# Optimization experiments

Hardware: AMD Instinct MI355X
Metric: run time of the kernel (lower is better)

Reference implementation:

```python
import jax, jax.numpy as jnp
import numpy as np

BETA = 0.001  # commitment loss weight from __init__ default


def setup_inputs() -> dict:
    key = jax.random.key(0)
    k1, k2 = jax.random.split(key)
    N, INPUT_DIM = 8192, 1024
    S, K, D = 32, 1024, 32  # nsplits, num_embeddings, embedding_dim
    z = jax.random.normal(k1, (N, INPUT_DIM), dtype=jnp.float32)
    # Stacked codebook weights: one [K, D] embedding table per split.
    W = jax.random.normal(k2, (S, K, D), dtype=jnp.float32)
    return {"z": z, "W": W}


def reference(z, W):
    N, INPUT_DIM = z.shape
    S, K, D = W.shape
    zc = z.reshape(N, S, D)  # per-split chunks, matches torch.chunk(z, S, -1)
    # Squared euclidean distances ||z||^2 + ||w||^2 - 2 z.w  -> [N, S, K]
    d2 = (
        jnp.sum(zc * zc, axis=-1, keepdims=True)
        + jnp.sum(W * W, axis=-1)[None, :, :]
        - 2.0 * jnp.einsum("nsd,skd->nsk", zc, W)
    )
    idx = jnp.argmin(d2, axis=-1)  # [N, S]
    # Gather nearest codes: W[s, idx[n, s]] -> [N, S, D]
    zq = W[jnp.arange(S)[None, :], idx]
    # Sum over splits of per-split mse means; equal split sizes so this is
    # S * mean over the whole tensor.
    sg = jax.lax.stop_gradient
    loss = S * (
        jnp.mean((sg(zq) - zc) ** 2) + BETA * jnp.mean((zq - sg(zc)) ** 2)
    )
    # Straight-through estimator
    zq_st = zc + sg(zq - zc)
    return zq_st.reshape(N, INPUT_DIM), loss
```

## Files before the change

kernel.cpp:

```cpp
#include <hip/hip_runtime.h>
#include <math.h>

#define NN 8192
#define SS 32
#define DD 32
#define KK 1024
#define OUT_ELEMS ((size_t)NN * SS * DD)

#define LOSS_SCALE (32.0f * 1.001f / 8388608.0f)

typedef _Float16 half8 __attribute__((ext_vector_type(8)));
typedef float   floatx4 __attribute__((ext_vector_type(4)));


__global__ __launch_bounds__(256) void vq_prep(const float* __restrict__ W,
                                               _Float16* __restrict__ wh,
                                               _Float16* __restrict__ wl,
                                               float* __restrict__ w2,
                                               float* __restrict__ out) {
    const int g    = blockIdx.x * 256 + threadIdx.x;
    const int row  = g >> 2;
    const int part = g & 3;
    const float* wr = W + (size_t)row * DD + part * 8;
    const float4 a = ((const float4*)wr)[0];
    const float4 b = ((const float4*)wr)[1];
    float ps = 0.0f;
    ps = fmaf(a.x, a.x, ps); ps = fmaf(a.y, a.y, ps);
    ps = fmaf(a.z, a.z, ps); ps = fmaf(a.w, a.w, ps);
    ps = fmaf(b.x, b.x, ps); ps = fmaf(b.y, b.y, ps);
    ps = fmaf(b.z, b.z, ps); ps = fmaf(b.w, b.w, ps);
    ps += __shfl_xor(ps, 1, 64);
    ps += __shfl_xor(ps, 2, 64);
    if (part == 0) w2[row] = ps;

    const float src[8] = {a.x, a.y, a.z, a.w, b.x, b.y, b.z, b.w};
    half8 h, l;
    #pragma unroll
    for (int j = 0; j < 8; ++j) {
        const _Float16 hv = (_Float16)src[j];
        h[j] = hv;
        l[j] = (_Float16)(src[j] - (float)hv);
    }
    *(half8*)(wh + (size_t)row * DD + part * 8) = h;
    *(half8*)(wl + (size_t)row * DD + part * 8) = l;
    if (g == 0) out[OUT_ELEMS] = 0.0f;
}

#define RG 4

__global__ __launch_bounds__(256, 4) void vq_mfma(const float* __restrict__ z,
                                                  const float* __restrict__ W,
                                                  const _Float16* __restrict__ wh,
                                                  const _Float16* __restrict__ wl,
                                                  const float* __restrict__ w2,
                                                  float* __restrict__ out) {
    __shared__ float lds_w2[KK + 16];
    __shared__ int   lds_idx[4][64];

    const int s    = blockIdx.x & (SS - 1);
    const int n0b  = (blockIdx.x >> 5) * 256;
    const int tid  = threadIdx.x;
    const int wv   = tid >> 6;
    const int lane = tid & 63;
    const int col  = lane & 15;
    const int quad = lane >> 4;

    const float* w2s = w2 + (size_t)s * KK;
    #pragma unroll
    for (int j = 0; j < 4; ++j) lds_w2[tid + j * 256] = w2s[tid + j * 256];
    __syncthreads();

    const int n0w = n0b + wv * 64;

    half8 zh[RG], zl[RG];
    #pragma unroll
    for (int rg = 0; rg < RG; ++rg) {
        const float* zp = z + (size_t)(n0w + rg * 16 + col) * (SS * DD) + s * DD + quad * 8;
        const float4 va = ((const float4*)zp)[0];
        const float4 vb = ((const float4*)zp)[1];
        const float src[8] = {va.x, va.y, va.z, va.w, vb.x, vb.y, vb.z, vb.w};
        #pragma unroll
        for (int j = 0; j < 8; ++j) {
            const float v = -2.0f * src[j];
            const _Float16 h = (_Float16)v;
            zh[rg][j] = h;
            zl[rg][j] = (_Float16)(v - (float)h);
        }
    }

    const _Float16* whs = wh + ((size_t)s * KK + col) * DD + quad * 8;
    const _Float16* wls = wl + ((size_t)s * KK + col) * DD + quad * 8;

    floatx4 best[RG];
    int bi[RG][4];
    #pragma unroll
    for (int rg = 0; rg < RG; ++rg) {
        best[rg] = (floatx4){INFINITY, INFINITY, INFINITY, INFINITY};
        bi[rg][0] = bi[rg][1] = bi[rg][2] = bi[rg][3] = 0;
    }

    half8 bh = *(const half8*)(whs);
    half8 bl = *(const half8*)(wls);
    float wv2 = lds_w2[col];

    for (int t = 0; t < KK / 16; ++t) {
        const half8 bh_n = *(const half8*)(whs + (size_t)(t + 1) * 16 * DD);
        const half8 bl_n = *(const half8*)(wls + (size_t)(t + 1) * 16 * DD);
        const float wv2_n = lds_w2[(t + 1) * 16 + col];

        #pragma unroll
        for (int rg = 0; rg < RG; ++rg) {
            floatx4 acc = {wv2, wv2, wv2, wv2};
            acc = __builtin_amdgcn_mfma_f32_16x16x32_f16(zh[rg], bh, acc, 0, 0, 0);
            acc = __builtin_amdgcn_mfma_f32_16x16x32_f16(zl[rg], bh, acc, 0, 0, 0);
            acc = __builtin_amdgcn_mfma_f32_16x16x32_f16(zh[rg], bl, acc, 0, 0, 0);
            #pragma unroll
            for (int i = 0; i < 4; ++i) {
                if (acc[i] < best[rg][i]) { best[rg][i] = acc[i]; bi[rg][i] = t; }
            }
        }
        bh = bh_n; bl = bl_n; wv2 = wv2_n;
    }

    #pragma unroll
    for (int rg = 0; rg < RG; ++rg) {
        #pragma unroll
        for (int i = 0; i < 4; ++i) {
            float v = best[rg][i];
            int   k = bi[rg][i] * 16 + col;
            #pragma unroll
            for (int m = 1; m < 16; m <<= 1) {
                const float vo = __shfl_xor(v, m, 64);
                const int   ko = __shfl_xor(k, m, 64);
                if (vo < v || (vo == v && ko < k)) { v = vo; k = ko; }
            }
            if (col == 0) lds_idx[wv][rg * 16 + quad * 4 + i] = k;
        }
    }
    __syncthreads();

    const int krow = lds_idx[wv][lane];
    const float* wsrc = W + ((size_t)s * KK + krow) * DD;
    const size_t zoff = (size_t)(n0w + lane) * (SS * DD) + s * DD;
    const float* zsrc = z + zoff;
    float* od = out + zoff;
    float sq = 0.0f;
    #pragma unroll
    for (int c = 0; c < 8; ++c) {
        const float4 wq = ((const float4*)wsrc)[c];
        const float4 zv = ((const float4*)zsrc)[c];
        const float d0 = wq.x - zv.x, d1 = wq.y - zv.y;
        const float d2 = wq.z - zv.z, d3 = wq.w - zv.w;
        sq = fmaf(d0, d0, sq); sq = fmaf(d1, d1, sq);
        sq = fmaf(d2, d2, sq); sq = fmaf(d3, d3, sq);
        ((float4*)od)[c] = wq;
    }
    #pragma unroll
    for (int off = 32; off > 0; off >>= 1) sq += __shfl_down(sq, off, 64);
    if (lane == 0) atomicAdd(out + OUT_ELEMS, sq * LOSS_SCALE);
}

extern "C" void kernel_launch(void* const* d_in, const int* in_sizes, int n_in,
                              void* d_out, int out_size, void* d_ws, size_t ws_size,
                              hipStream_t stream) {
    const float* z = (const float*)d_in[0];
    const float* W = (const float*)d_in[1];
    float* out = (float*)d_out;

    _Float16* wh = (_Float16*)d_ws;
    _Float16* wl = wh + (size_t)SS * KK * DD;
    float*    w2 = (float*)(wl + (size_t)SS * KK * DD);

    vq_prep<<<dim3((SS * KK * 4) / 256), dim3(256), 0, stream>>>(W, wh, wl, w2, out);
    vq_mfma<<<dim3((NN / 256) * SS), dim3(256), 0, stream>>>(z, W, wh, wl, w2, out);
}
```

Before: 176.9 us.

## Fuse codebook fp16 split conversion into main kernel with LDS double buffering

Removes the separate prep kernel and performs the fp16 hi/lo split and squared-norm computation on the fly inside the main kernel. Each block stages 64-code chunks through double-buffered shared memory, so the four waves share one conversion per chunk, and a barrier follows each chunk. The loss accumulator is now zeroed with a memset. This drops one launch and the workspace round trip. In exchange, every block redoes the conversion of its split's codebook, each chunk adds a barrier, and the occupancy hint falls from 4 to 2 blocks.

Result: no change. 174.5 us (-1.3%).

```diff
diff --git a/kernel.cpp b/kernel.cpp
--- a/kernel.cpp
+++ b/kernel.cpp
@@ -12,50 +12,17 @@
 typedef _Float16 half8 __attribute__((ext_vector_type(8)));
 typedef float   floatx4 __attribute__((ext_vector_type(4)));
 
+#define CH_TILES 4
+#define CHUNK_K  (CH_TILES * 16)
+#define NCHUNK   (KK / CHUNK_K)
 
-__global__ __launch_bounds__(256) void vq_prep(const float* __restrict__ W,
-                                               _Float16* __restrict__ wh,
-                                               _Float16* __restrict__ wl,
-                                               float* __restrict__ w2,
-                                               float* __restrict__ out) {
-    const int g    = blockIdx.x * 256 + threadIdx.x;
-    const int row  = g >> 2;
-    const int part = g & 3;
-    const float* wr = W + (size_t)row * DD + part * 8;
-    const float4 a = ((const float4*)wr)[0];
-    const float4 b = ((const float4*)wr)[1];
-    float ps = 0.0f;
-    ps = fmaf(a.x, a.x, ps); ps = fmaf(a.y, a.y, ps);
-    ps = fmaf(a.z, a.z, ps); ps = fmaf(a.w, a.w, ps);
-    ps = fmaf(b.x, b.x, ps); ps = fmaf(b.y, b.y, ps);
-    ps = fmaf(b.z, b.z, ps); ps = fmaf(b.w, b.w, ps);
-    ps += __shfl_xor(ps, 1, 64);
-    ps += __shfl_xor(ps, 2, 64);
-    if (part == 0) w2[row] = ps;
-
-    const float src[8] = {a.x, a.y, a.z, a.w, b.x, b.y, b.z, b.w};
-    half8 h, l;
-    #pragma unroll
-    for (int j = 0; j < 8; ++j) {
-        const _Float16 hv = (_Float16)src[j];
-        h[j] = hv;
-        l[j] = (_Float16)(src[j] - (float)hv);
-    }
-    *(half8*)(wh + (size_t)row * DD + part * 8) = h;
-    *(half8*)(wl + (size_t)row * DD + part * 8) = l;
-    if (g == 0) out[OUT_ELEMS] = 0.0f;
-}
-
-#define RG 4
-
-__global__ __launch_bounds__(256, 4) void vq_mfma(const float* __restrict__ z,
-                                                  const float* __restrict__ W,
-                                                  const _Float16* __restrict__ wh,
-                                                  const _Float16* __restrict__ wl,
-                                                  const float* __restrict__ w2,
-                                                  float* __restrict__ out) {
-    __shared__ float lds_w2[KK + 16];
-    __shared__ int   lds_idx[4][64];
+__global__ __launch_bounds__(256, 2) void vq_fused(const float* __restrict__ z,
+                                                   const float* __restrict__ W,
+                                                   float* __restrict__ out) {
+    __shared__ _Float16 bufH[2][CH_TILES][64][8];
+    __shared__ _Float16 bufL[2][CH_TILES][64][8];
+    __shared__ float    w2b[2][CHUNK_K];
+    __shared__ int      lds_idx[4][64];
 
     const int s    = blockIdx.x & (SS - 1);
     const int n0b  = (blockIdx.x >> 5) * 256;
@@ -65,16 +32,12 @@
     const int col  = lane & 15;
     const int quad = lane >> 4;
 
-    const float* w2s = w2 + (size_t)s * KK;
-    #pragma unroll
-    for (int j = 0; j < 4; ++j) lds_w2[tid + j * 256] = w2s[tid + j * 256];
-    __syncthreads();
-
+    const float* __restrict__ Ws = W + (size_t)s * KK * DD;
     const int n0w = n0b + wv * 64;
 
-    half8 zh[RG], zl[RG];
+    half8 zh[4], zl[4];
     #pragma unroll
-    for (int rg = 0; rg < RG; ++rg) {
+    for (int rg = 0; rg < 4; ++rg) {
         const float* zp = z + (size_t)(n0w + rg * 16 + col) * (SS * DD) + s * DD + quad * 8;
         const float4 va = ((const float4*)zp)[0];
         const float4 vb = ((const float4*)zp)[1];
@@ -88,42 +51,87 @@
         }
     }
 
-    const _Float16* whs = wh + ((size_t)s * KK + col) * DD + quad * 8;
-    const _Float16* wls = wl + ((size_t)s * KK + col) * DD + quad * 8;
+    const float* __restrict__ stg = Ws + ((size_t)(wv * 16 + col)) * DD + quad * 8;
 
-    floatx4 best[RG];
-    int bi[RG][4];
+    floatx4 best[4];
+    int bi[4][4];
     #pragma unroll
-    for (int rg = 0; rg < RG; ++rg) {
+    for (int rg = 0; rg < 4; ++rg) {
         best[rg] = (floatx4){INFINITY, INFINITY, INFINITY, INFINITY};
         bi[rg][0] = bi[rg][1] = bi[rg][2] = bi[rg][3] = 0;
     }
 
-    half8 bh = *(const half8*)(whs);
-    half8 bl = *(const half8*)(wls);
-    float wv2 = lds_w2[col];
+    float4 pa = ((const float4*)stg)[0];
+    float4 pb = ((const float4*)stg)[1];
+    {
+        const float src[8] = {pa.x, pa.y, pa.z, pa.w, pb.x, pb.y, pb.z, pb.w};
+        half8 h8, l8; float ps = 0.0f;
+        #pragma unroll
+        for (int j = 0; j < 8; ++j) {
+            const float v = src[j];
+            ps = fmaf(v, v, ps);
+            const _Float16 h = (_Float16)v;
+            h8[j] = h;
+            l8[j] = (_Float16)(v - (float)h);
+        }
+        ps += __shfl_xor(ps, 16, 64);
+        ps += __shfl_xor(ps, 32, 64);
+        *(half8*)&bufH[0][wv][lane][0] = h8;
+        *(half8*)&bufL[0][wv][lane][0] = l8;
+        if (quad == 0) w2b[0][wv * 16 + col] = ps;
+    }
+    __syncthreads();
 
-    for (int t = 0; t < KK / 16; ++t) {
-        const half8 bh_n = *(const half8*)(whs + (size_t)(t + 1) * 16 * DD);
-        const half8 bl_n = *(const half8*)(wls + (size_t)(t + 1) * 16 * DD);
-        const float wv2_n = lds_w2[(t + 1) * 16 + col];
+    for (int c = 0; c < NCHUNK; ++c) {
+        const int b = c & 1;
+        if (c + 1 < NCHUNK) {
+            const float* nsrc = stg + (size_t)(c + 1) * CHUNK_K * DD;
+            pa = ((const float4*)nsrc)[0];
+            pb = ((const float4*)nsrc)[1];
+        }
 
         #pragma unroll
-        for (int rg = 0; rg < RG; ++rg) {
-            floatx4 acc = {wv2, wv2, wv2, wv2};
-            acc = __builtin_amdgcn_mfma_f32_16x16x32_f16(zh[rg], bh, acc, 0, 0, 0);
-            acc = __builtin_amdgcn_mfma_f32_16x16x32_f16(zl[rg], bh, acc, 0, 0, 0);
-            acc = __builtin_amdgcn_mfma_f32_16x16x32_f16(zh[rg], bl, acc, 0, 0, 0);
+        for (int tt = 0; tt < CH_TILES; ++tt) {
+            const half8 bh = *(const half8*)&bufH[b][tt][lane][0];
+            const half8 bl = *(const half8*)&bufL[b][tt][lane][0];
+            const float wv2 = w2b[b][tt * 16 + col];
+            const floatx4 c0 = {wv2, wv2, wv2, wv2};
+            const int tk = c * CH_TILES + tt;
             #pragma unroll
-            for (int i = 0; i < 4; ++i) {
-                if (acc[i] < best[rg][i]) { best[rg][i] = acc[i]; bi[rg][i] = t; }
+            for (int rg = 0; rg < 4; ++rg) {
+                floatx4 acc = __builtin_amdgcn_mfma_f32_16x16x32_f16(zh[rg], bh, c0, 0, 0, 0);
+                acc = __builtin_amdgcn_mfma_f32_16x16x32_f16(zl[rg], bh, acc, 0, 0, 0);
+                acc = __builtin_amdgcn_mfma_f32_16x16x32_f16(zh[rg], bl, acc, 0, 0, 0);
+                #pragma unroll
+                for (int i = 0; i < 4; ++i) {
+                    if (acc[i] < best[rg][i]) { best[rg][i] = acc[i]; bi[rg][i] = tk; }
+                }
             }
         }
-        bh = bh_n; bl = bl_n; wv2 = wv2_n;
+
+        if (c + 1 < NCHUNK) {
+            const float src[8] = {pa.x, pa.y, pa.z, pa.w, pb.x, pb.y, pb.z, pb.w};
+            half8 h8, l8; float ps = 0.0f;
+            #pragma unroll
+            for (int j = 0; j < 8; ++j) {
+                const float v = src[j];
+                ps = fmaf(v, v, ps);
+                const _Float16 h = (_Float16)v;
+                h8[j] = h;
+                l8[j] = (_Float16)(v - (float)h);
+            }
+            ps += __shfl_xor(ps, 16, 64);
+            ps += __shfl_xor(ps, 32, 64);
+            const int nb = (c + 1) & 1;
+            *(half8*)&bufH[nb][wv][lane][0] = h8;
+            *(half8*)&bufL[nb][wv][lane][0] = l8;
+            if (quad == 0) w2b[nb][wv * 16 + col] = ps;
+            __syncthreads();
+        }
     }
 
     #pragma unroll
-    for (int rg = 0; rg < RG; ++rg) {
+    for (int rg = 0; rg < 4; ++rg) {
         #pragma unroll
         for (int i = 0; i < 4; ++i) {
             float v = best[rg][i];
@@ -140,20 +148,20 @@
     __syncthreads();
 
     const int krow = lds_idx[wv][lane];
-    const float* wsrc = W + ((size_t)s * KK + krow) * DD;
+    const float* wsrc = Ws + (size_t)krow * DD;
     const size_t zoff = (size_t)(n0w + lane) * (SS * DD) + s * DD;
     const float* zsrc = z + zoff;
     float* od = out + zoff;
     float sq = 0.0f;
     #pragma unroll
-    for (int c = 0; c < 8; ++c) {
-        const float4 wq = ((const float4*)wsrc)[c];
-        const float4 zv = ((const float4*)zsrc)[c];
+    for (int cc = 0; cc < 8; ++cc) {
+        const float4 wq = ((const float4*)wsrc)[cc];
+        const float4 zv = ((const float4*)zsrc)[cc];
         const float d0 = wq.x - zv.x, d1 = wq.y - zv.y;
         const float d2 = wq.z - zv.z, d3 = wq.w - zv.w;
         sq = fmaf(d0, d0, sq); sq = fmaf(d1, d1, sq);
         sq = fmaf(d2, d2, sq); sq = fmaf(d3, d3, sq);
-        ((float4*)od)[c] = wq;
+        ((float4*)od)[cc] = wq;
     }
     #pragma unroll
     for (int off = 32; off > 0; off >>= 1) sq += __shfl_down(sq, off, 64);
@@ -167,10 +175,6 @@
     const float* W = (const float*)d_in[1];
     float* out = (float*)d_out;
 
-    _Float16* wh = (_Float16*)d_ws;
-    _Float16* wl = wh + (size_t)SS * KK * DD;
-    float*    w2 = (float*)(wl + (size_t)SS * KK * DD);
-
-    vq_prep<<<dim3((SS * KK * 4) / 256), dim3(256), 0, stream>>>(W, wh, wl, w2, out);
-    vq_mfma<<<dim3((NN / 256) * SS), dim3(256), 0, stream>>>(z, W, wh, wl, w2, out);
+    hipMemsetAsync((char*)out + OUT_ELEMS * sizeof(float), 0, sizeof(float), stream);
+    vq_fused<<<dim3((NN / 256) * SS), dim3(256), 0, stream>>>(z, W, out);
 }
```
